# Optimization experiments

Hardware: AMD Instinct MI355X
Metric: run time of the kernel (lower is better)

## Reference

```python
import jax, jax.numpy as jnp
import numpy as np

DIM = 512
HEADS = 8
HEAD_DIM = DIM // HEADS
SCALE = HEAD_DIM ** -0.5
CPB_HIDDEN = 512
N_CLASSES = 2
LN_EPS = 1e-5


def _layernorm(x, g, b):
    m = jnp.mean(x, axis=-1, keepdims=True)
    v = jnp.var(x, axis=-1, keepdims=True)
    return (x - m) / jnp.sqrt(v + LN_EPS) * g + b


def _coord_attention(x, coords, cpb_w1, cpb_b1, cpb_w2, cpb_b2, qkv_w, qkv_b, proj_w, proj_b):
    B, N, C = x.shape
    qkv = (x @ qkv_w + qkv_b).reshape(B, N, 3, HEADS, HEAD_DIM)
    q, k, v = jnp.moveaxis(qkv, 2, 0)  # each (B, N, H, hd)
    attn = jnp.einsum('bnhd,bmhd->bhnm', q * SCALE, k)  # (B, H, N, N)
    rel = coords[:, :, None, :] - coords[:, None, :, :]  # (B, N, N, 2)
    rel = rel / (jnp.linalg.norm(rel, axis=-1, keepdims=True) + 1e-6)
    bias = jax.nn.relu(rel @ cpb_w1 + cpb_b1) @ cpb_w2 + cpb_b2  # (B, N, N, H)
    attn = jax.nn.softmax(attn + jnp.transpose(bias, (0, 3, 1, 2)), axis=-1)
    out = jnp.einsum('bhnm,bmhd->bnhd', attn, v).reshape(B, N, C)
    return out @ proj_w + proj_b


def setup_inputs() -> dict:
    key = jax.random.key(0)
    ks = iter(jax.random.split(key, 32))
    d = {}
    d['h'] = jax.random.normal(next(ks), (1, 400, 1024), dtype=jnp.float32)
    d['coords'] = jax.random.uniform(next(ks), (1, 400, 2), dtype=jnp.float32) * 1000.0
    def lin(kw, kb, fan_in, fan_out):
        w = jax.random.normal(kw, (fan_in, fan_out), dtype=jnp.float32) / np.sqrt(fan_in)
        b = jax.random.normal(kb, (fan_out,), dtype=jnp.float32) * 0.01
        return w, b
    d['fc1_w'], d['fc1_b'] = lin(next(ks), next(ks), 1024, DIM)
    d['cls_token'] = jax.random.normal(next(ks), (1, 1, DIM), dtype=jnp.float32)
    for p in ('l1', 'l2'):
        d[p + '_norm_g'] = jnp.ones((DIM,), jnp.float32)
        d[p + '_norm_b'] = jnp.zeros((DIM,), jnp.float32)
        d[p + '_cpb_w1'], d[p + '_cpb_b1'] = lin(next(ks), next(ks), 2, CPB_HIDDEN)
        d[p + '_cpb_w2'], d[p + '_cpb_b2'] = lin(next(ks), next(ks), CPB_HIDDEN, HEADS)
        d[p + '_qkv_w'], d[p + '_qkv_b'] = lin(next(ks), next(ks), DIM, 3 * DIM)
        d[p + '_proj_w'], d[p + '_proj_b'] = lin(next(ks), next(ks), DIM, DIM)
    d['norm_g'] = jnp.ones((DIM,), jnp.float32)
    d['norm_b'] = jnp.zeros((DIM,), jnp.float32)
    d['fc2_w'], d['fc2_b'] = lin(next(ks), next(ks), DIM, N_CLASSES)
    return d


def reference(h, coords, fc1_w, fc1_b, cls_token,
              l1_norm_g, l1_norm_b, l1_cpb_w1, l1_cpb_b1, l1_cpb_w2, l1_cpb_b2,
              l1_qkv_w, l1_qkv_b, l1_proj_w, l1_proj_b,
              l2_norm_g, l2_norm_b, l2_cpb_w1, l2_cpb_b1, l2_cpb_w2, l2_cpb_b2,
              l2_qkv_w, l2_qkv_b, l2_proj_w, l2_proj_b,
              norm_g, norm_b, fc2_w, fc2_b):
    B, Np, _ = h.shape
    h = jax.nn.relu(h @ fc1_w + fc1_b)  # (B, N, 512)
    side = int(np.ceil(np.sqrt(Np)))
    add = side * side - Np  # pad bag to a perfect square (wrap-around copy)
    h = jnp.concatenate([h, h[:, :add, :]], axis=1)
    coords = jnp.concatenate([coords, coords[:, :add, :]], axis=1)
    cls = jnp.broadcast_to(cls_token, (B, 1, DIM))
    h = jnp.concatenate([cls, h], axis=1)
    coords = jnp.concatenate([jnp.zeros((B, 1, 2), h.dtype), coords], axis=1)
    h = h + _coord_attention(_layernorm(h, l1_norm_g, l1_norm_b), coords,
                             l1_cpb_w1, l1_cpb_b1, l1_cpb_w2, l1_cpb_b2,
                             l1_qkv_w, l1_qkv_b, l1_proj_w, l1_proj_b)
    h = h + _coord_attention(_layernorm(h, l2_norm_g, l2_norm_b), coords,
                             l2_cpb_w1, l2_cpb_b1, l2_cpb_w2, l2_cpb_b2,
                             l2_qkv_w, l2_qkv_b, l2_proj_w, l2_proj_b)
    h = _layernorm(h, norm_g, norm_b)[:, 0]  # CLS token
    return h @ fc2_w + fc2_b  # (B, n_classes)
```

## Files before the change

kernel.cpp:

```cpp
#include <hip/hip_runtime.h>
#include <math.h>

#define NP 401
#define DIM 512
#define LN_EPS 1e-5f
#define ATT_SCALE 0.125f
#define SP 448
#define PLANE (NP * SP)
#define CPB_M 16384
#define TSTRIDE (CPB_M + 64)
#define PQS (401L * 1536)
#define PVS (401L * 512)

template<bool TB, typename LA, typename LB>
__device__ __forceinline__ void gemm64(
    int kBeg, int kEnd, int tid,
    float (*as)[68], float (*bs)[68], float (&acc)[4][4],
    LA&& loadA, LB&& loadB)
{
    float aR[4], bR[4];
    loadA(kBeg, aR);
    loadB(kBeg, bR);
    for (int k0 = kBeg; k0 < kEnd; k0 += 16) {
        const int arow = tid >> 2, aq = tid & 3;
        as[aq * 4 + 0][arow] = aR[0];
        as[aq * 4 + 1][arow] = aR[1];
        as[aq * 4 + 2][arow] = aR[2];
        as[aq * 4 + 3][arow] = aR[3];
        if (!TB) {
            *(float4*)&bs[tid >> 4][(tid & 15) * 4] =
                make_float4(bR[0], bR[1], bR[2], bR[3]);
        } else {
            bs[aq * 4 + 0][arow] = bR[0];
            bs[aq * 4 + 1][arow] = bR[1];
            bs[aq * 4 + 2][arow] = bR[2];
            bs[aq * 4 + 3][arow] = bR[3];
        }
        __syncthreads();
        float nA[4] = {0.f,0.f,0.f,0.f}, nB[4] = {0.f,0.f,0.f,0.f};
        if (k0 + 16 < kEnd) { loadA(k0 + 16, nA); loadB(k0 + 16, nB); }
        const int tx = tid & 15, ty = tid >> 4;
        #pragma unroll
        for (int kk = 0; kk < 16; ++kk) {
            float4 a4 = *(const float4*)&as[kk][ty * 4];
            float4 b4 = *(const float4*)&bs[kk][tx * 4];
            float av[4] = {a4.x, a4.y, a4.z, a4.w};
            float bv[4] = {b4.x, b4.y, b4.z, b4.w};
            #pragma unroll
            for (int r = 0; r < 4; ++r)
                #pragma unroll
                for (int c = 0; c < 4; ++c)
                    acc[r][c] = fmaf(av[r], bv[c], acc[r][c]);
        }
        __syncthreads();
        #pragma unroll
        for (int j = 0; j < 4; ++j) { aR[j] = nA[j]; bR[j] = nB[j]; }
    }
}

__global__ __launch_bounds__(256) void gemm_split_kernel(
    const float* __restrict__ A, int lda,
    const float* __restrict__ B, int ldb,
    float* __restrict__ P, int ldc, long slice,
    int M, int N, int K, int skN)
{
    __shared__ float as[16][68], bs[16][68];
    const int tid = threadIdx.x;
    const int m0 = blockIdx.x * 64, n0 = blockIdx.y * 64;
    const int sk = blockIdx.z;
    const int KS = ((K + skN * 16 - 1) / (skN * 16)) * 16;
    const int kBeg = sk * KS;
    const int kEnd = (kBeg + KS < K) ? kBeg + KS : K;
    float acc[4][4] = {};

    auto loadA = [&](int k0, float r[4]) {
        r[0] = r[1] = r[2] = r[3] = 0.f;
        int gm = m0 + (tid >> 2);
        if (gm >= M) return;
        int gk = k0 + (tid & 3) * 4;
        const float* p = A + (long)gm * lda + gk;
        if (gk + 3 < kEnd) {
            float4 v = *(const float4*)p;
            r[0] = v.x; r[1] = v.y; r[2] = v.z; r[3] = v.w;
        } else {
            #pragma unroll
            for (int j = 0; j < 4; ++j) if (gk + j < kEnd) r[j] = p[j];
        }
    };
    auto loadB = [&](int k0, float r[4]) {
        r[0] = r[1] = r[2] = r[3] = 0.f;
        int gk = k0 + (tid >> 4);
        if (gk >= kEnd) return;
        int gn = n0 + (tid & 15) * 4;
        const float* p = B + (long)gk * ldb + gn;
        float4 v = *(const float4*)p;
        r[0] = v.x; r[1] = v.y; r[2] = v.z; r[3] = v.w;
    };
    if (kBeg < kEnd)
        gemm64<false>(kBeg, kEnd, tid, as, bs, acc, loadA, loadB);

    float* C = P + (long)sk * slice;
    const int tx = tid & 15, ty = tid >> 4;
    #pragma unroll
    for (int r = 0; r < 4; ++r) {
        int m = m0 + ty * 4 + r;
        if (m >= M) continue;
        *(float4*)&C[(long)m * ldc + n0 + tx * 4] =
            make_float4(acc[r][0], acc[r][1], acc[r][2], acc[r][3]);
    }
}

__global__ __launch_bounds__(256) void reduce_kernel(
    const float* __restrict__ P, long slice, int skN,
    const float* __restrict__ bias, float* __restrict__ out,
    int total, int N)
{
    int idx = (blockIdx.x * 256 + threadIdx.x) * 4;
    if (idx >= total) return;
    float4 s = *(const float4*)(P + idx);
    for (int k = 1; k < skN; ++k) {
        float4 p = *(const float4*)(P + (long)k * slice + idx);
        s.x += p.x; s.y += p.y; s.z += p.z; s.w += p.w;
    }
    if (bias) {
        const float4 b = *(const float4*)(bias + (idx % N));
        s.x += b.x; s.y += b.y; s.z += b.z; s.w += b.w;
    }
    *(float4*)(out + idx) = s;
}

__global__ __launch_bounds__(256) void qk_kernel(
    const float* __restrict__ qkv,
    const int* __restrict__ pm, const float* __restrict__ pf,
    const float* __restrict__ T, float* __restrict__ S)
{
    __shared__ float as[16][68], bs[16][68];
    const int tid = threadIdx.x;
    const int m0 = blockIdx.x * 64, n0 = blockIdx.y * 64, h = blockIdx.z;
    float acc[4][4] = {};

    auto loadQ = [&](int k0, float r[4]) {
        int gm = m0 + (tid >> 2);
        if (gm > 400) { r[0]=r[1]=r[2]=r[3]=0.f; return; }
        int gk = k0 + (tid & 3) * 4;
        float4 v = *(const float4*)(qkv + (long)gm * 1536 + h * 64 + gk);
        r[0]=v.x; r[1]=v.y; r[2]=v.z; r[3]=v.w;
    };
    auto loadK = [&](int k0, float r[4]) {
        int gn = n0 + (tid >> 2);
        if (gn > 400) { r[0]=r[1]=r[2]=r[3]=0.f; return; }
        int gk = k0 + (tid & 3) * 4;
        float4 v = *(const float4*)(qkv + (long)gn * 1536 + 512 + h * 64 + gk);
        r[0]=v.x; r[1]=v.y; r[2]=v.z; r[3]=v.w;
    };
    gemm64<true>(0, 64, tid, as, bs, acc, loadQ, loadK);

    const int tx = tid & 15, ty = tid >> 4;
    const float* Tt = T + (long)h * TSTRIDE;
    float* Sp = S + (long)h * PLANE;
    #pragma unroll
    for (int r = 0; r < 4; ++r) {
        int i = m0 + ty * 4 + r;
        if (i > 400) continue;
        #pragma unroll
        for (int c = 0; c < 4; ++c) {
            int j = n0 + tx * 4 + c;
            if (j > 400) continue;
            int id = i * 416 + j;
            int mm = pm[id];
            float fr = pf[id];
            float t0 = Tt[mm], t1 = Tt[mm + 1];
            Sp[(long)i * SP + j] =
                fmaf(acc[r][c], ATT_SCALE, fmaf(fr, t1 - t0, t0));
        }
    }
}

__global__ __launch_bounds__(256) void softmax_kernel(float* __restrict__ S)
{
    int r = blockIdx.x * 4 + (threadIdx.x >> 6);
    if (r >= 3208) return;
    int hh = r / 401, i = r - hh * 401;
    float* row = S + (long)hh * PLANE + (long)i * SP;
    int lane = threadIdx.x & 63;
    float v[7], mx = -INFINITY;
    #pragma unroll
    for (int j = 0; j < 7; ++j) {
        int c = lane + j * 64;
        v[j] = (c < NP) ? row[c] : -INFINITY;
        mx = fmaxf(mx, v[j]);
    }
    #pragma unroll
    for (int off = 32; off > 0; off >>= 1)
        mx = fmaxf(mx, __shfl_xor(mx, off));
    float s = 0.f;
    #pragma unroll
    for (int j = 0; j < 7; ++j) {
        v[j] = (lane + j * 64 < NP) ? __expf(v[j] - mx) : 0.f;
        s += v[j];
    }
    #pragma unroll
    for (int off = 32; off > 0; off >>= 1)
        s += __shfl_xor(s, off);
    float inv = 1.f / s;
    #pragma unroll
    for (int j = 0; j < 7; ++j) {
        int c = lane + j * 64;
        if (c < NP) row[c] = v[j] * inv;
    }
}

__global__ __launch_bounds__(256) void pv_kernel(
    const float* __restrict__ S, const float* __restrict__ qkv,
    float* __restrict__ Pv)
{
    __shared__ float as[16][68], bs[16][68];
    const int tid = threadIdx.x;
    const int m0 = blockIdx.x * 64;
    const int h = blockIdx.z >> 2, sk = blockIdx.z & 3;
    const int kBeg = sk * 112;
    const int kEnd = (kBeg + 112 < NP) ? kBeg + 112 : NP;
    float acc[4][4] = {};

    auto loadA = [&](int k0, float r[4]) {
        r[0] = r[1] = r[2] = r[3] = 0.f;
        int gm = m0 + (tid >> 2);
        if (gm > 400) return;
        int gk = k0 + (tid & 3) * 4;
        const float* p = S + (long)h * PLANE + (long)gm * SP + gk;
        if (gk + 3 < kEnd) {
            float4 v = *(const float4*)p;
            r[0]=v.x; r[1]=v.y; r[2]=v.z; r[3]=v.w;
        } else {
            #pragma unroll
            for (int j = 0; j < 4; ++j) if (gk + j < kEnd) r[j] = p[j];
        }
    };
    auto loadB = [&](int k0, float r[4]) {
        r[0] = r[1] = r[2] = r[3] = 0.f;
        int key = k0 + (tid >> 4);
        if (key >= kEnd) return;
        int d = (tid & 15) * 4;
        float4 v = *(const float4*)(qkv + (long)key * 1536 + 1024 + h * 64 + d);
        r[0]=v.x; r[1]=v.y; r[2]=v.z; r[3]=v.w;
    };
    gemm64<false>(kBeg, kEnd, tid, as, bs, acc, loadA, loadB);

    float* C = Pv + (long)sk * PVS;
    const int tx = tid & 15, ty = tid >> 4;
    #pragma unroll
    for (int r = 0; r < 4; ++r) {
        int m = m0 + ty * 4 + r;
        if (m > 400) continue;
        *(float4*)&C[(long)m * 512 + h * 64 + tx * 4] =
            make_float4(acc[r][0], acc[r][1], acc[r][2], acc[r][3]);
    }
}

__global__ __launch_bounds__(256) void proj_kernel(
    const float* __restrict__ att, const float* __restrict__ projw,
    float* __restrict__ Pp)
{
    __shared__ float as[16][68], bs[16][68];
    const int tid = threadIdx.x;
    const int m0 = blockIdx.x * 64, n0 = blockIdx.y * 64, sk = blockIdx.z;
    const int kBeg = sk * 64, kEnd = kBeg + 64;
    float acc[4][4] = {};

    auto loadA = [&](int k0, float r[4]) {
        r[0] = r[1] = r[2] = r[3] = 0.f;
        int gm = m0 + (tid >> 2);
        if (gm > 400) return;
        int gk = k0 + (tid & 3) * 4;
        float4 v = *(const float4*)(att + (long)gm * 512 + gk);
        r[0]=v.x; r[1]=v.y; r[2]=v.z; r[3]=v.w;
    };
    auto loadB = [&](int k0, float r[4]) {
        int gk = k0 + (tid >> 4);
        int gn = n0 + (tid & 15) * 4;
        float4 v = *(const float4*)(projw + (long)gk * 512 + gn);
        r[0]=v.x; r[1]=v.y; r[2]=v.z; r[3]=v.w;
    };
    gemm64<false>(kBeg, kEnd, tid, as, bs, acc, loadA, loadB);

    float* C = Pp + (long)sk * PVS;
    const int tx = tid & 15, ty = tid >> 4;
    #pragma unroll
    for (int r = 0; r < 4; ++r) {
        int m = m0 + ty * 4 + r;
        if (m > 400) continue;
        *(float4*)&C[(long)m * 512 + n0 + tx * 4] =
            make_float4(acc[r][0], acc[r][1], acc[r][2], acc[r][3]);
    }
}

__global__ __launch_bounds__(256) void rowfuse_kernel(
    const float* __restrict__ P, long slice, int skN, int rowOff,
    const float* __restrict__ bias, int doRelu,
    const float* __restrict__ resid, const float* __restrict__ cls,
    float* __restrict__ h0,
    const float* __restrict__ g, const float* __restrict__ b,
    float* __restrict__ xln)
{
    const int r = blockIdx.x, t = threadIdx.x;
    float v0, v1;
    if (cls && r == 0) {
        v0 = cls[t]; v1 = cls[t + 256];
    } else {
        const float* p = P + (long)(r - rowOff) * DIM;
        v0 = bias[t]; v1 = bias[t + 256];
        for (int k = 0; k < skN; ++k) {
            v0 += p[(long)k * slice + t];
            v1 += p[(long)k * slice + t + 256];
        }
        if (resid) {
            v0 += resid[(long)r * DIM + t];
            v1 += resid[(long)r * DIM + t + 256];
        }
        if (doRelu) { v0 = fmaxf(v0, 0.f); v1 = fmaxf(v1, 0.f); }
    }
    h0[(long)r * DIM + t] = v0;
    h0[(long)r * DIM + t + 256] = v1;

    float s = v0 + v1, sq = v0 * v0 + v1 * v1;
    #pragma unroll
    for (int off = 32; off > 0; off >>= 1) {
        s += __shfl_down(s, off);
        sq += __shfl_down(sq, off);
    }
    __shared__ float ps[4], pq[4];
    int w = t >> 6, lane = t & 63;
    if (lane == 0) { ps[w] = s; pq[w] = sq; }
    __syncthreads();
    float Sm = ps[0] + ps[1] + ps[2] + ps[3];
    float Q = pq[0] + pq[1] + pq[2] + pq[3];
    float mean = Sm * (1.f / DIM);
    float var = Q * (1.f / DIM) - mean * mean;
    float inv = rsqrtf(var + LN_EPS);
    xln[(long)r * DIM + t]       = (v0 - mean) * inv * g[t] + b[t];
    xln[(long)r * DIM + t + 256] = (v1 - mean) * inv * g[t + 256] + b[t + 256];
}

__global__ __launch_bounds__(256) void cls_decode_kernel(
    const float* __restrict__ qkv,
    const int* __restrict__ pm, const float* __restrict__ pf,
    const float* __restrict__ T,
    float* __restrict__ cms, float* __restrict__ cpv)
{
    const int h = blockIdx.x, c = blockIdx.y, tid = threadIdx.x;
    const int kBeg = c * 64;
    __shared__ float q0[64], scraw[64], p[64], red[4][64], rr[2];

    if (tid < 64) q0[tid] = qkv[h * 64 + tid];
    __syncthreads();

    {
        int k = tid >> 2, q = tid & 3;
        int j = kBeg + k;
        float dot = 0.f;
        if (j < NP) {
            const float* kp = qkv + (long)j * 1536 + 512 + h * 64 + q * 16;
            const float* qp = q0 + q * 16;
            #pragma unroll
            for (int d = 0; d < 16; d += 4) {
                float4 kv = *(const float4*)(kp + d);
                float4 qq = *(const float4*)(qp + d);
                dot = fmaf(qq.x, kv.x, dot);
                dot = fmaf(qq.y, kv.y, dot);
                dot = fmaf(qq.z, kv.z, dot);
                dot = fmaf(qq.w, kv.w, dot);
            }
        }
        dot += __shfl_down(dot, 2);
        dot += __shfl_down(dot, 1);
        if (q == 0) scraw[k] = dot;
    }
    __syncthreads();

    if (tid < 64) {
        int j = kBeg + tid;
        float s;
        if (j < NP) {
            int mm = pm[j];
            float fr = pf[j];
            const float* Tt = T + (long)h * TSTRIDE;
            float t0 = Tt[mm], t1 = Tt[mm + 1];
            s = fmaf(scraw[tid], ATT_SCALE, fmaf(fr, t1 - t0, t0));
        } else {
            s = -INFINITY;
        }
        float m = s;
        #pragma unroll
        for (int off = 32; off > 0; off >>= 1)
            m = fmaxf(m, __shfl_xor(m, off));
        float e = (j < NP) ? __expf(s - m) : 0.f;
        float sum = e;
        #pragma unroll
        for (int off = 32; off > 0; off >>= 1)
            sum += __shfl_xor(sum, off);
        p[tid] = e;
        if (tid == 0) { rr[0] = m; rr[1] = sum; }
    }
    __syncthreads();

    {
        int w = tid >> 6, d = tid & 63;
        float acc = 0.f;
        for (int k = w; k < 64; k += 4) {
            int j = kBeg + k;
            if (j >= NP) break;
            acc = fmaf(p[k], qkv[(long)j * 1536 + 1024 + h * 64 + d], acc);
        }
        red[w][d] = acc;
    }
    __syncthreads();
    if (tid < 64) {
        cpv[((long)h * 7 + c) * 64 + tid] =
            red[0][tid] + red[1][tid] + red[2][tid] + red[3][tid];
        if (tid == 0) {
            cms[(h * 7 + c) * 2 + 0] = rr[0];
            cms[(h * 7 + c) * 2 + 1] = rr[1];
        }
    }
}

__global__ __launch_bounds__(256) void cls_proj_kernel(
    const float* __restrict__ cms, const float* __restrict__ cpv,
    const float* __restrict__ projw, const float* __restrict__ projb,
    float* __restrict__ proj0)
{
    __shared__ float av[512], red[4][64];
    const int b = blockIdx.x, tid = threadIdx.x;
    for (int d = tid; d < 512; d += 256) {
        int h = d >> 6, dd = d & 63;
        float M = -INFINITY;
        #pragma unroll
        for (int c = 0; c < 7; ++c)
            M = fmaxf(M, cms[(h * 7 + c) * 2]);
        float S = 0.f, acc = 0.f;
        #pragma unroll
        for (int c = 0; c < 7; ++c) {
            float e = __expf(cms[(h * 7 + c) * 2] - M);
            S += cms[(h * 7 + c) * 2 + 1] * e;
            acc += cpv[((long)h * 7 + c) * 64 + dd] * e;
        }
        av[d] = acc / S;
    }
    __syncthreads();
    int g = tid >> 6, n = b * 64 + (tid & 63);
    float acc = 0.f;
    for (int k = g * 128; k < g * 128 + 128; ++k)
        acc = fmaf(av[k], projw[(long)k * 512 + n], acc);
    red[g][tid & 63] = acc;
    __syncthreads();
    if (tid < 64)
        proj0[b * 64 + tid] = red[0][tid] + red[1][tid] + red[2][tid]
                              + red[3][tid] + projb[b * 64 + tid];
}

__global__ __launch_bounds__(256) void cls_out_kernel(
    const float* __restrict__ h0, const float* __restrict__ proj0,
    const float* __restrict__ g, const float* __restrict__ b,
    const float* __restrict__ fc2w, const float* __restrict__ fc2b,
    float* __restrict__ out)
{
    const int t = threadIdx.x;
    float v0 = h0[t] + proj0[t];
    float v1 = h0[t + 256] + proj0[t + 256];
    float s = v0 + v1, sq = v0 * v0 + v1 * v1;
    #pragma unroll
    for (int off = 32; off > 0; off >>= 1) {
        s += __shfl_down(s, off);
        sq += __shfl_down(sq, off);
    }
    __shared__ float ps[4], pq[4], pc0[4], pc1[4];
    int w = t >> 6, lane = t & 63;
    if (lane == 0) { ps[w] = s; pq[w] = sq; }
    __syncthreads();
    float Sm = ps[0] + ps[1] + ps[2] + ps[3];
    float Q = pq[0] + pq[1] + pq[2] + pq[3];
    float mean = Sm * (1.f / DIM);
    float var = Q * (1.f / DIM) - mean * mean;
    float inv = rsqrtf(var + LN_EPS);
    float n0 = (v0 - mean) * inv * g[t] + b[t];
    float n1 = (v1 - mean) * inv * g[t + 256] + b[t + 256];
    float c0 = n0 * fc2w[t * 2]     + n1 * fc2w[(t + 256) * 2];
    float c1 = n0 * fc2w[t * 2 + 1] + n1 * fc2w[(t + 256) * 2 + 1];
    #pragma unroll
    for (int off = 32; off > 0; off >>= 1) {
        c0 += __shfl_down(c0, off);
        c1 += __shfl_down(c1, off);
    }
    if (lane == 0) { pc0[w] = c0; pc1[w] = c1; }
    __syncthreads();
    if (t == 0) {
        out[0] = pc0[0] + pc0[1] + pc0[2] + pc0[3] + fc2b[0];
        out[1] = pc1[0] + pc1[1] + pc1[2] + pc1[3] + fc2b[1];
    }
}

__global__ __launch_bounds__(256) void mega_kernel(
    const float* __restrict__ hin, const float* __restrict__ fc1_w,
    const float* __restrict__ w1_0, const float* __restrict__ b1_0,
    const float* __restrict__ w2_0, const float* __restrict__ b2_0,
    const float* __restrict__ w1_1, const float* __restrict__ b1_1,
    const float* __restrict__ w2_1, const float* __restrict__ b2_1,
    const float* __restrict__ coords,
    float* __restrict__ Pp, float* __restrict__ T,
    int* __restrict__ pm, float* __restrict__ pf)
{
    __shared__ float smem[2176];
    float (*as)[68] = (float(*)[68])smem;
    float (*bs)[68] = (float(*)[68])(smem + 1088);
    float (*red)[64][8] = (float(*)[64][8])smem;
    const int bid = blockIdx.x, tid = threadIdx.x;

    if (bid < 896) {
        int sk = bid / 56, rem = bid % 56;
        int m0 = (rem % 7) * 64, n0 = (rem / 7) * 64;
        int kBeg = sk * 64, kEnd = kBeg + 64;
        float acc[4][4] = {};
        auto loadA = [&](int k0, float r[4]) {
            r[0]=r[1]=r[2]=r[3]=0.f;
            int gm = m0 + (tid >> 2);
            if (gm >= 400) return;
            int gk = k0 + (tid & 3) * 4;
            float4 v = *(const float4*)(hin + (long)gm * 1024 + gk);
            r[0]=v.x; r[1]=v.y; r[2]=v.z; r[3]=v.w;
        };
        auto loadB = [&](int k0, float r[4]) {
            int gk = k0 + (tid >> 4);
            int gn = n0 + (tid & 15) * 4;
            float4 v = *(const float4*)(fc1_w + (long)gk * 512 + gn);
            r[0]=v.x; r[1]=v.y; r[2]=v.z; r[3]=v.w;
        };
        gemm64<false>(kBeg, kEnd, tid, as, bs, acc, loadA, loadB);
        float* C = Pp + (long)sk * PVS;
        const int tx = tid & 15, ty = tid >> 4;
        #pragma unroll
        for (int r = 0; r < 4; ++r) {
            int m = m0 + ty * 4 + r;
            if (m >= 400) continue;
            *(float4*)&C[(long)m * 512 + n0 + tx * 4] =
                make_float4(acc[r][0], acc[r][1], acc[r][2], acc[r][3]);
        }
    } else if (bid < 1410) {
        int tb = bid - 896;
        int z = tb / 257, ab = tb % 257;
        const float* w1 = z ? w1_1 : w1_0;
        const float* b1 = z ? b1_1 : b1_0;
        const float* w2 = z ? w2_1 : w2_0;
        const float* b2 = z ? b2_1 : b2_0;
        const int lane = tid & 63, wv = tid >> 6;
        float ca = 0.f, sa = 0.f;
        if (ab != 256) {
            float th = fmaf((float)(ab * 64 + lane),
                            (float)(2.0 * M_PI / CPB_M), -(float)M_PI);
            sincosf(th, &sa, &ca);
        } else if (lane == 0) {
            sincosf((float)M_PI, &sa, &ca);
        }
        float a8[8] = {};
        const int kbeg = wv * 128;
        #pragma unroll 4
        for (int k = kbeg; k < kbeg + 128; ++k) {
            float hk = fmaxf(fmaf(ca, w1[k],
                                  fmaf(sa, w1[512 + k], b1[k])), 0.f);
            #pragma unroll
            for (int h2 = 0; h2 < 8; ++h2)
                a8[h2] = fmaf(hk, w2[k * 8 + h2], a8[h2]);
        }
        #pragma unroll
        for (int h2 = 0; h2 < 8; ++h2) red[wv][lane][h2] = a8[h2];
        __syncthreads();
        if (tid < 64) {
            int aidx = ab * 64 + tid;
            #pragma unroll
            for (int h2 = 0; h2 < 8; ++h2)
                T[(long)(z * 8 + h2) * TSTRIDE + aidx] =
                    red[0][tid][h2] + red[1][tid][h2] +
                    red[2][tid][h2] + red[3][tid][h2] + b2[h2];
        }
    } else {
        int p = (bid - 1410) * 256 + tid;
        if (p < NP * NP) {
            int i = p / NP, j = p - i * NP;
            float xi = (i == 0) ? 0.f : coords[(i - 1) * 2];
            float yi = (i == 0) ? 0.f : coords[(i - 1) * 2 + 1];
            float xj = (j == 0) ? 0.f : coords[(j - 1) * 2];
            float yj = (j == 0) ? 0.f : coords[(j - 1) * 2 + 1];
            float rx = xi - xj, ry = yi - yj;
            int mm; float fr;
            if (rx == 0.f && ry == 0.f) {
                mm = CPB_M + 1; fr = 0.f;
            } else {
                float x = (atan2f(ry, rx) + 3.14159265358979f)
                          * (float)(CPB_M / (2.0 * M_PI));
                int mi = (int)x;
                fr = x - (float)mi;
                mm = (mi >= CPB_M) ? mi - CPB_M : mi;
            }
            pm[i * 416 + j] = mm;
            pf[i * 416 + j] = fr;
        }
    }
}

extern "C" void kernel_launch(void* const* d_in, const int* in_sizes, int n_in,
                              void* d_out, int out_size, void* d_ws, size_t ws_size,
                              hipStream_t stream)
{
    const float* coords = (const float*)d_in[1];
    float* ws = (float*)d_ws;
    float* h0   = ws;                    ws += 401L * 512;
    float* xln  = ws;                    ws += 401L * 512;
    float* S    = ws;                    ws += 8L * PLANE;
    float* T    = ws;                    ws += 16L * TSTRIDE;
    int*   pm   = (int*)ws;              ws += 401L * 416;
    float* pf   = ws;                    ws += 401L * 416;
    float* Pq   = ws;                    ws += 4L * PQS;
    float* qkv  = ws;                    ws += 401L * 1536;
    float* Pv   = ws;                    ws += 4L * PVS;
    float* att  = ws;                    ws += 401L * 512;
    float* Pp   = ws;                    ws += 16L * PVS;
    float* proj0 = ws;                   ws += 512;
    float* cms  = ws;                    ws += 8L * 7 * 2;
    float* cpv  = ws;                    ws += 8L * 7 * 64;

    mega_kernel<<<2039, 256, 0, stream>>>(
        (const float*)d_in[0], (const float*)d_in[2],
        (const float*)d_in[7],  (const float*)d_in[8],
        (const float*)d_in[9],  (const float*)d_in[10],
        (const float*)d_in[17], (const float*)d_in[18],
        (const float*)d_in[19], (const float*)d_in[20],
        coords, Pp, T, pm, pf);

    rowfuse_kernel<<<401, 256, 0, stream>>>(
        Pp, PVS, 16, 1, (const float*)d_in[3], 1, nullptr,
        (const float*)d_in[4], h0,
        (const float*)d_in[5], (const float*)d_in[6], xln);

    gemm_split_kernel<<<dim3(7, 24, 4), 256, 0, stream>>>(
        xln, 512, (const float*)d_in[11], 1536, Pq, 1536, PQS,
        401, 1536, 512, 4);
    reduce_kernel<<<602, 256, 0, stream>>>(
        Pq, PQS, 4, (const float*)d_in[12], qkv, 401 * 1536, 1536);
    qk_kernel<<<dim3(7, 7, 8), 256, 0, stream>>>(qkv, pm, pf, T, S);
    softmax_kernel<<<802, 256, 0, stream>>>(S);
    pv_kernel<<<dim3(7, 1, 32), 256, 0, stream>>>(S, qkv, Pv);
    reduce_kernel<<<201, 256, 0, stream>>>(
        Pv, PVS, 4, nullptr, att, 401 * 512, 512);
    proj_kernel<<<dim3(7, 8, 8), 256, 0, stream>>>(
        att, (const float*)d_in[13], Pp);
    rowfuse_kernel<<<401, 256, 0, stream>>>(
        Pp, PVS, 8, 0, (const float*)d_in[14], 0, h0, nullptr, h0,
        (const float*)d_in[15], (const float*)d_in[16], xln);

    gemm_split_kernel<<<dim3(7, 24, 4), 256, 0, stream>>>(
        xln, 512, (const float*)d_in[21], 1536, Pq, 1536, PQS,
        401, 1536, 512, 4);
    reduce_kernel<<<602, 256, 0, stream>>>(
        Pq, PQS, 4, (const float*)d_in[22], qkv, 401 * 1536, 1536);
    cls_decode_kernel<<<dim3(8, 7), 256, 0, stream>>>(
        qkv, pm, pf, T + 8L * TSTRIDE, cms, cpv);
    cls_proj_kernel<<<8, 256, 0, stream>>>(
        cms, cpv, (const float*)d_in[23], (const float*)d_in[24], proj0);
    cls_out_kernel<<<1, 256, 0, stream>>>(
        h0, proj0, (const float*)d_in[25], (const float*)d_in[26],
        (const float*)d_in[27], (const float*)d_in[28], (float*)d_out);
}
```

Baseline: 250.4 us.

## Fuse layer-1 attention into flash-style kernel and merge CLS tail kernels

Replaces the separate QK, softmax, split-K PV and reduce kernels of the first attention layer with one online-softmax flash kernel. Each block handles 32 queries for one head, streams K/V tiles through shared memory and writes normalized output directly, so the score matrix and the PV partials never go to global memory. The three CLS-only kernels for the second layer are merged into one single-block kernel that loops over heads and then does projection, layernorm and classifier. This cuts launches and memory traffic, but the flash grid has only 104 blocks and the tail runs serially on one block, so parallelism drops.

```diff
diff --git a/kernel.cpp b/kernel.cpp
--- a/kernel.cpp
+++ b/kernel.cpp
@@ -5,8 +5,6 @@
 #define DIM 512
 #define LN_EPS 1e-5f
 #define ATT_SCALE 0.125f
-#define SP 448
-#define PLANE (NP * SP)
 #define CPB_M 16384
 #define TSTRIDE (CPB_M + 64)
 #define PQS (401L * 1536)
@@ -129,131 +127,162 @@
     *(float4*)(out + idx) = s;
 }
 
-__global__ __launch_bounds__(256) void qk_kernel(
+__global__ __launch_bounds__(256) void flash_kernel(
     const float* __restrict__ qkv,
     const int* __restrict__ pm, const float* __restrict__ pf,
-    const float* __restrict__ T, float* __restrict__ S)
-{
-    __shared__ float as[16][68], bs[16][68];
+    const float* __restrict__ T, float* __restrict__ att)
+{
+    __shared__ float qsT[64 * 32];
+    __shared__ float kT[64 * 68];
+    __shared__ float vs[64 * 68];
+    __shared__ float psT[64 * 34];
     const int tid = threadIdx.x;
-    const int m0 = blockIdx.x * 64, n0 = blockIdx.y * 64, h = blockIdx.z;
-    float acc[4][4] = {};
-
-    auto loadQ = [&](int k0, float r[4]) {
-        int gm = m0 + (tid >> 2);
-        if (gm > 400) { r[0]=r[1]=r[2]=r[3]=0.f; return; }
-        int gk = k0 + (tid & 3) * 4;
-        float4 v = *(const float4*)(qkv + (long)gm * 1536 + h * 64 + gk);
-        r[0]=v.x; r[1]=v.y; r[2]=v.z; r[3]=v.w;
-    };
-    auto loadK = [&](int k0, float r[4]) {
-        int gn = n0 + (tid >> 2);
-        if (gn > 400) { r[0]=r[1]=r[2]=r[3]=0.f; return; }
-        int gk = k0 + (tid & 3) * 4;
-        float4 v = *(const float4*)(qkv + (long)gn * 1536 + 512 + h * 64 + gk);
-        r[0]=v.x; r[1]=v.y; r[2]=v.z; r[3]=v.w;
-    };
-    gemm64<true>(0, 64, tid, as, bs, acc, loadQ, loadK);
-
+    const int m0 = blockIdx.x * 32, h = blockIdx.y;
     const int tx = tid & 15, ty = tid >> 4;
+    const int i0 = ty * 2;
+
+    {
+        int i = tid >> 3, dq = (tid & 7) * 8;
+        int gm = m0 + i;
+        float4 a = make_float4(0, 0, 0, 0), b = make_float4(0, 0, 0, 0);
+        if (gm <= 400) {
+            const float* p = qkv + (long)gm * 1536 + h * 64 + dq;
+            a = *(const float4*)p;
+            b = *(const float4*)(p + 4);
+        }
+        qsT[(dq + 0) * 32 + i] = a.x;
+        qsT[(dq + 1) * 32 + i] = a.y;
+        qsT[(dq + 2) * 32 + i] = a.z;
+        qsT[(dq + 3) * 32 + i] = a.w;
+        qsT[(dq + 4) * 32 + i] = b.x;
+        qsT[(dq + 5) * 32 + i] = b.y;
+        qsT[(dq + 6) * 32 + i] = b.z;
+        qsT[(dq + 7) * 32 + i] = b.w;
+    }
+
+    float O[2][4] = {{0.f,0.f,0.f,0.f},{0.f,0.f,0.f,0.f}};
+    float mr[2] = {-INFINITY, -INFINITY};
+    float lr[2] = {0.f, 0.f};
     const float* Tt = T + (long)h * TSTRIDE;
-    float* Sp = S + (long)h * PLANE;
+    const int ig0 = (m0 + i0     <= 400) ? m0 + i0     : 400;
+    const int ig1 = (m0 + i0 + 1 <= 400) ? m0 + i0 + 1 : 400;
+
+    for (int c = 0; c < 7; ++c) {
+        const int kBeg = c * 64;
+        __syncthreads();
+        {
+            int j = tid >> 2, dq = (tid & 3) * 16;
+            int gj = kBeg + j;
+            float4 k4[4], v4[4];
+            #pragma unroll
+            for (int q = 0; q < 4; ++q) {
+                k4[q] = make_float4(0, 0, 0, 0);
+                v4[q] = make_float4(0, 0, 0, 0);
+            }
+            if (gj <= 400) {
+                const float* kp = qkv + (long)gj * 1536 + 512 + h * 64 + dq;
+                const float* vp = kp + 512;
+                #pragma unroll
+                for (int q = 0; q < 4; ++q) {
+                    k4[q] = *(const float4*)(kp + q * 4);
+                    v4[q] = *(const float4*)(vp + q * 4);
+                }
+            }
+            #pragma unroll
+            for (int q = 0; q < 4; ++q) {
+                kT[(dq + q * 4 + 0) * 68 + j] = k4[q].x;
+                kT[(dq + q * 4 + 1) * 68 + j] = k4[q].y;
+                kT[(dq + q * 4 + 2) * 68 + j] = k4[q].z;
+                kT[(dq + q * 4 + 3) * 68 + j] = k4[q].w;
+                *(float4*)&vs[j * 68 + dq + q * 4] = v4[q];
+            }
+        }
+        __syncthreads();
+
+        float s0[4] = {0.f,0.f,0.f,0.f}, s1[4] = {0.f,0.f,0.f,0.f};
+        #pragma unroll
+        for (int d = 0; d < 64; ++d) {
+            float2 q2 = *(const float2*)&qsT[d * 32 + i0];
+            float4 k4 = *(const float4*)&kT[d * 68 + tx * 4];
+            s0[0] = fmaf(q2.x, k4.x, s0[0]);
+            s0[1] = fmaf(q2.x, k4.y, s0[1]);
+            s0[2] = fmaf(q2.x, k4.z, s0[2]);
+            s0[3] = fmaf(q2.x, k4.w, s0[3]);
+            s1[0] = fmaf(q2.y, k4.x, s1[0]);
+            s1[1] = fmaf(q2.y, k4.y, s1[1]);
+            s1[2] = fmaf(q2.y, k4.z, s1[2]);
+            s1[3] = fmaf(q2.y, k4.w, s1[3]);
+        }
+        #pragma unroll
+        for (int cc = 0; cc < 4; ++cc) {
+            int jg = kBeg + tx * 4 + cc;
+            if (jg <= 400) {
+                int id0 = ig0 * 416 + jg, id1 = ig1 * 416 + jg;
+                int ma = pm[id0], mb = pm[id1];
+                float fa = pf[id0], fb = pf[id1];
+                float a0 = Tt[ma], a1 = Tt[ma + 1];
+                float b0 = Tt[mb], b1 = Tt[mb + 1];
+                s0[cc] = fmaf(s0[cc], ATT_SCALE, fmaf(fa, a1 - a0, a0));
+                s1[cc] = fmaf(s1[cc], ATT_SCALE, fmaf(fb, b1 - b0, b0));
+            } else {
+                s0[cc] = -INFINITY;
+                s1[cc] = -INFINITY;
+            }
+        }
+        #pragma unroll
+        for (int r = 0; r < 2; ++r) {
+            float* s = r ? s1 : s0;
+            float cmax = fmaxf(fmaxf(s[0], s[1]), fmaxf(s[2], s[3]));
+            cmax = fmaxf(cmax, __shfl_xor(cmax, 1));
+            cmax = fmaxf(cmax, __shfl_xor(cmax, 2));
+            cmax = fmaxf(cmax, __shfl_xor(cmax, 4));
+            cmax = fmaxf(cmax, __shfl_xor(cmax, 8));
+            float mn = fmaxf(mr[r], cmax);
+            float al = __expf(mr[r] - mn);
+            float rs = 0.f;
+            #pragma unroll
+            for (int cc = 0; cc < 4; ++cc) {
+                float e = __expf(s[cc] - mn);
+                s[cc] = e;
+                rs += e;
+            }
+            rs += __shfl_xor(rs, 1);
+            rs += __shfl_xor(rs, 2);
+            rs += __shfl_xor(rs, 4);
+            rs += __shfl_xor(rs, 8);
+            lr[r] = lr[r] * al + rs;
+            mr[r] = mn;
+            #pragma unroll
+            for (int cc = 0; cc < 4; ++cc) {
+                O[r][cc] *= al;
+                psT[(tx * 4 + cc) * 34 + i0 + r] = s[cc];
+            }
+        }
+        __syncthreads();
+
+        #pragma unroll 4
+        for (int j = 0; j < 64; ++j) {
+            float2 p2 = *(const float2*)&psT[j * 34 + i0];
+            float4 v4 = *(const float4*)&vs[j * 68 + tx * 4];
+            O[0][0] = fmaf(p2.x, v4.x, O[0][0]);
+            O[0][1] = fmaf(p2.x, v4.y, O[0][1]);
+            O[0][2] = fmaf(p2.x, v4.z, O[0][2]);
+            O[0][3] = fmaf(p2.x, v4.w, O[0][3]);
+            O[1][0] = fmaf(p2.y, v4.x, O[1][0]);
+            O[1][1] = fmaf(p2.y, v4.y, O[1][1]);
+            O[1][2] = fmaf(p2.y, v4.z, O[1][2]);
+            O[1][3] = fmaf(p2.y, v4.w, O[1][3]);
+        }
+    }
+
     #pragma unroll
-    for (int r = 0; r < 4; ++r) {
-        int i = m0 + ty * 4 + r;
-        if (i > 400) continue;
-        #pragma unroll
-        for (int c = 0; c < 4; ++c) {
-            int j = n0 + tx * 4 + c;
-            if (j > 400) continue;
-            int id = i * 416 + j;
-            int mm = pm[id];
-            float fr = pf[id];
-            float t0 = Tt[mm], t1 = Tt[mm + 1];
-            Sp[(long)i * SP + j] =
-                fmaf(acc[r][c], ATT_SCALE, fmaf(fr, t1 - t0, t0));
-        }
-    }
-}
-
-__global__ __launch_bounds__(256) void softmax_kernel(float* __restrict__ S)
-{
-    int r = blockIdx.x * 4 + (threadIdx.x >> 6);
-    if (r >= 3208) return;
-    int hh = r / 401, i = r - hh * 401;
-    float* row = S + (long)hh * PLANE + (long)i * SP;
-    int lane = threadIdx.x & 63;
-    float v[7], mx = -INFINITY;
-    #pragma unroll
-    for (int j = 0; j < 7; ++j) {
-        int c = lane + j * 64;
-        v[j] = (c < NP) ? row[c] : -INFINITY;
-        mx = fmaxf(mx, v[j]);
-    }
-    #pragma unroll
-    for (int off = 32; off > 0; off >>= 1)
-        mx = fmaxf(mx, __shfl_xor(mx, off));
-    float s = 0.f;
-    #pragma unroll
-    for (int j = 0; j < 7; ++j) {
-        v[j] = (lane + j * 64 < NP) ? __expf(v[j] - mx) : 0.f;
-        s += v[j];
-    }
-    #pragma unroll
-    for (int off = 32; off > 0; off >>= 1)
-        s += __shfl_xor(s, off);
-    float inv = 1.f / s;
-    #pragma unroll
-    for (int j = 0; j < 7; ++j) {
-        int c = lane + j * 64;
-        if (c < NP) row[c] = v[j] * inv;
-    }
-}
-
-__global__ __launch_bounds__(256) void pv_kernel(
-    const float* __restrict__ S, const float* __restrict__ qkv,
-    float* __restrict__ Pv)
-{
-    __shared__ float as[16][68], bs[16][68];
-    const int tid = threadIdx.x;
-    const int m0 = blockIdx.x * 64;
-    const int h = blockIdx.z >> 2, sk = blockIdx.z & 3;
-    const int kBeg = sk * 112;
-    const int kEnd = (kBeg + 112 < NP) ? kBeg + 112 : NP;
-    float acc[4][4] = {};
-
-    auto loadA = [&](int k0, float r[4]) {
-        r[0] = r[1] = r[2] = r[3] = 0.f;
-        int gm = m0 + (tid >> 2);
-        if (gm > 400) return;
-        int gk = k0 + (tid & 3) * 4;
-        const float* p = S + (long)h * PLANE + (long)gm * SP + gk;
-        if (gk + 3 < kEnd) {
-            float4 v = *(const float4*)p;
-            r[0]=v.x; r[1]=v.y; r[2]=v.z; r[3]=v.w;
-        } else {
-            #pragma unroll
-            for (int j = 0; j < 4; ++j) if (gk + j < kEnd) r[j] = p[j];
-        }
-    };
-    auto loadB = [&](int k0, float r[4]) {
-        r[0] = r[1] = r[2] = r[3] = 0.f;
-        int key = k0 + (tid >> 4);
-        if (key >= kEnd) return;
-        int d = (tid & 15) * 4;
-        float4 v = *(const float4*)(qkv + (long)key * 1536 + 1024 + h * 64 + d);
-        r[0]=v.x; r[1]=v.y; r[2]=v.z; r[3]=v.w;
-    };
-    gemm64<false>(kBeg, kEnd, tid, as, bs, acc, loadA, loadB);
-
-    float* C = Pv + (long)sk * PVS;
-    const int tx = tid & 15, ty = tid >> 4;
-    #pragma unroll
-    for (int r = 0; r < 4; ++r) {
-        int m = m0 + ty * 4 + r;
-        if (m > 400) continue;
-        *(float4*)&C[(long)m * 512 + h * 64 + tx * 4] =
-            make_float4(acc[r][0], acc[r][1], acc[r][2], acc[r][3]);
+    for (int r = 0; r < 2; ++r) {
+        int ig = m0 + i0 + r;
+        if (ig > 400) continue;
+        float inv = 1.f / lr[r];
+        *(float4*)&att[(long)ig * 512 + h * 64 + tx * 4] =
+            make_float4(O[r][0] * inv, O[r][1] * inv,
+                        O[r][2] * inv, O[r][3] * inv);
     }
 }
 
@@ -341,132 +370,86 @@
     xln[(long)r * DIM + t + 256] = (v1 - mean) * inv * g[t + 256] + b[t + 256];
 }
 
-__global__ __launch_bounds__(256) void cls_decode_kernel(
+__global__ __launch_bounds__(256) void cls_tail_kernel(
     const float* __restrict__ qkv,
     const int* __restrict__ pm, const float* __restrict__ pf,
     const float* __restrict__ T,
-    float* __restrict__ cms, float* __restrict__ cpv)
-{
-    const int h = blockIdx.x, c = blockIdx.y, tid = threadIdx.x;
-    const int kBeg = c * 64;
-    __shared__ float q0[64], scraw[64], p[64], red[4][64], rr[2];
-
-    if (tid < 64) q0[tid] = qkv[h * 64 + tid];
-    __syncthreads();
-
-    {
-        int k = tid >> 2, q = tid & 3;
-        int j = kBeg + k;
-        float dot = 0.f;
-        if (j < NP) {
-            const float* kp = qkv + (long)j * 1536 + 512 + h * 64 + q * 16;
-            const float* qp = q0 + q * 16;
-            #pragma unroll
-            for (int d = 0; d < 16; d += 4) {
-                float4 kv = *(const float4*)(kp + d);
-                float4 qq = *(const float4*)(qp + d);
-                dot = fmaf(qq.x, kv.x, dot);
-                dot = fmaf(qq.y, kv.y, dot);
-                dot = fmaf(qq.z, kv.z, dot);
-                dot = fmaf(qq.w, kv.w, dot);
-            }
-        }
-        dot += __shfl_down(dot, 2);
-        dot += __shfl_down(dot, 1);
-        if (q == 0) scraw[k] = dot;
-    }
-    __syncthreads();
-
-    if (tid < 64) {
-        int j = kBeg + tid;
-        float s;
-        if (j < NP) {
-            int mm = pm[j];
-            float fr = pf[j];
-            const float* Tt = T + (long)h * TSTRIDE;
-            float t0 = Tt[mm], t1 = Tt[mm + 1];
-            s = fmaf(scraw[tid], ATT_SCALE, fmaf(fr, t1 - t0, t0));
-        } else {
-            s = -INFINITY;
-        }
-        float m = s;
-        #pragma unroll
-        for (int off = 32; off > 0; off >>= 1)
-            m = fmaxf(m, __shfl_xor(m, off));
-        float e = (j < NP) ? __expf(s - m) : 0.f;
-        float sum = e;
-        #pragma unroll
-        for (int off = 32; off > 0; off >>= 1)
-            sum += __shfl_xor(sum, off);
-        p[tid] = e;
-        if (tid == 0) { rr[0] = m; rr[1] = sum; }
-    }
-    __syncthreads();
-
-    {
-        int w = tid >> 6, d = tid & 63;
-        float acc = 0.f;
-        for (int k = w; k < 64; k += 4) {
-            int j = kBeg + k;
-            if (j >= NP) break;
-            acc = fmaf(p[k], qkv[(long)j * 1536 + 1024 + h * 64 + d], acc);
-        }
-        red[w][d] = acc;
-    }
-    __syncthreads();
-    if (tid < 64) {
-        cpv[((long)h * 7 + c) * 64 + tid] =
-            red[0][tid] + red[1][tid] + red[2][tid] + red[3][tid];
-        if (tid == 0) {
-            cms[(h * 7 + c) * 2 + 0] = rr[0];
-            cms[(h * 7 + c) * 2 + 1] = rr[1];
-        }
-    }
-}
-
-__global__ __launch_bounds__(256) void cls_proj_kernel(
-    const float* __restrict__ cms, const float* __restrict__ cpv,
     const float* __restrict__ projw, const float* __restrict__ projb,
-    float* __restrict__ proj0)
-{
-    __shared__ float av[512], red[4][64];
-    const int b = blockIdx.x, tid = threadIdx.x;
-    for (int d = tid; d < 512; d += 256) {
-        int h = d >> 6, dd = d & 63;
-        float M = -INFINITY;
-        #pragma unroll
-        for (int c = 0; c < 7; ++c)
-            M = fmaxf(M, cms[(h * 7 + c) * 2]);
-        float S = 0.f, acc = 0.f;
-        #pragma unroll
-        for (int c = 0; c < 7; ++c) {
-            float e = __expf(cms[(h * 7 + c) * 2] - M);
-            S += cms[(h * 7 + c) * 2 + 1] * e;
-            acc += cpv[((long)h * 7 + c) * 64 + dd] * e;
-        }
-        av[d] = acc / S;
-    }
-    __syncthreads();
-    int g = tid >> 6, n = b * 64 + (tid & 63);
-    float acc = 0.f;
-    for (int k = g * 128; k < g * 128 + 128; ++k)
-        acc = fmaf(av[k], projw[(long)k * 512 + n], acc);
-    red[g][tid & 63] = acc;
-    __syncthreads();
-    if (tid < 64)
-        proj0[b * 64 + tid] = red[0][tid] + red[1][tid] + red[2][tid]
-                              + red[3][tid] + projb[b * 64 + tid];
-}
-
-__global__ __launch_bounds__(256) void cls_out_kernel(
-    const float* __restrict__ h0, const float* __restrict__ proj0,
+    const float* __restrict__ h0,
     const float* __restrict__ g, const float* __restrict__ b,
     const float* __restrict__ fc2w, const float* __restrict__ fc2b,
     float* __restrict__ out)
 {
-    const int t = threadIdx.x;
-    float v0 = h0[t] + proj0[t];
-    float v1 = h0[t + 256] + proj0[t + 256];
+    const int tid = threadIdx.x;
+    const int w = tid >> 6, lane = tid & 63;
+    __shared__ float q0[64], sc[512], av[512], red[4][64], rr[8];
+
+    for (int h = 0; h < 8; ++h) {
+        if (tid < 64) q0[tid] = qkv[h * 64 + tid];
+        __syncthreads();
+        const float* Tt = T + (long)h * TSTRIDE;
+        #pragma unroll
+        for (int jj = 0; jj < 2; ++jj) {
+            int j = tid + jj * 256;
+            if (j < NP) {
+                const float* kp = qkv + (long)j * 1536 + 512 + h * 64;
+                float dot = 0.f;
+                #pragma unroll
+                for (int d = 0; d < 64; d += 4) {
+                    float4 kv = *(const float4*)(kp + d);
+                    float4 qq = *(const float4*)(q0 + d);
+                    dot = fmaf(qq.x, kv.x, dot);
+                    dot = fmaf(qq.y, kv.y, dot);
+                    dot = fmaf(qq.z, kv.z, dot);
+                    dot = fmaf(qq.w, kv.w, dot);
+                }
+                int mm = pm[j];
+                float fr = pf[j];
+                float t0 = Tt[mm], t1 = Tt[mm + 1];
+                sc[j] = fmaf(dot, ATT_SCALE, fmaf(fr, t1 - t0, t0));
+            } else if (j < 512) {
+                sc[j] = -INFINITY;
+            }
+        }
+        __syncthreads();
+        float mx = fmaxf(sc[tid], sc[tid + 256]);
+        #pragma unroll
+        for (int off = 32; off > 0; off >>= 1)
+            mx = fmaxf(mx, __shfl_xor(mx, off));
+        if (lane == 0) rr[w] = mx;
+        __syncthreads();
+        float M = fmaxf(fmaxf(rr[0], rr[1]), fmaxf(rr[2], rr[3]));
+        float e0 = (tid < NP) ? __expf(sc[tid] - M) : 0.f;
+        float e1 = (tid + 256 < NP) ? __expf(sc[tid + 256] - M) : 0.f;
+        float s = e0 + e1;
+        #pragma unroll
+        for (int off = 32; off > 0; off >>= 1)
+            s += __shfl_xor(s, off);
+        if (lane == 0) rr[4 + w] = s;
+        __syncthreads();
+        float inv = 1.f / (rr[4] + rr[5] + rr[6] + rr[7]);
+        sc[tid] = e0 * inv;
+        sc[tid + 256] = e1 * inv;
+        __syncthreads();
+        float acc = 0.f;
+        for (int j = w; j < NP; j += 4)
+            acc = fmaf(sc[j], qkv[(long)j * 1536 + 1024 + h * 64 + lane], acc);
+        red[w][lane] = acc;
+        __syncthreads();
+        if (tid < 64)
+            av[h * 64 + tid] =
+                red[0][tid] + red[1][tid] + red[2][tid] + red[3][tid];
+        __syncthreads();
+    }
+
+    float a0 = projb[tid], a1 = projb[tid + 256];
+    #pragma unroll 8
+    for (int k = 0; k < 512; ++k) {
+        float avk = av[k];
+        a0 = fmaf(avk, projw[(long)k * 512 + tid], a0);
+        a1 = fmaf(avk, projw[(long)k * 512 + tid + 256], a1);
+    }
+    float v0 = h0[tid] + a0, v1 = h0[tid + 256] + a1;
     float s = v0 + v1, sq = v0 * v0 + v1 * v1;
     #pragma unroll
     for (int off = 32; off > 0; off >>= 1) {
@@ -474,7 +457,6 @@
         sq += __shfl_down(sq, off);
     }
     __shared__ float ps[4], pq[4], pc0[4], pc1[4];
-    int w = t >> 6, lane = t & 63;
     if (lane == 0) { ps[w] = s; pq[w] = sq; }
     __syncthreads();
     float Sm = ps[0] + ps[1] + ps[2] + ps[3];
@@ -482,10 +464,10 @@
     float mean = Sm * (1.f / DIM);
     float var = Q * (1.f / DIM) - mean * mean;
     float inv = rsqrtf(var + LN_EPS);
-    float n0 = (v0 - mean) * inv * g[t] + b[t];
-    float n1 = (v1 - mean) * inv * g[t + 256] + b[t + 256];
-    float c0 = n0 * fc2w[t * 2]     + n1 * fc2w[(t + 256) * 2];
-    float c1 = n0 * fc2w[t * 2 + 1] + n1 * fc2w[(t + 256) * 2 + 1];
+    float n0 = (v0 - mean) * inv * g[tid] + b[tid];
+    float n1 = (v1 - mean) * inv * g[tid + 256] + b[tid + 256];
+    float c0 = n0 * fc2w[tid * 2]     + n1 * fc2w[(tid + 256) * 2];
+    float c1 = n0 * fc2w[tid * 2 + 1] + n1 * fc2w[(tid + 256) * 2 + 1];
     #pragma unroll
     for (int off = 32; off > 0; off >>= 1) {
         c0 += __shfl_down(c0, off);
@@ -493,7 +475,7 @@
     }
     if (lane == 0) { pc0[w] = c0; pc1[w] = c1; }
     __syncthreads();
-    if (t == 0) {
+    if (tid == 0) {
         out[0] = pc0[0] + pc0[1] + pc0[2] + pc0[3] + fc2b[0];
         out[1] = pc1[0] + pc1[1] + pc1[2] + pc1[3] + fc2b[1];
     }
@@ -614,18 +596,13 @@
     float* ws = (float*)d_ws;
     float* h0   = ws;                    ws += 401L * 512;
     float* xln  = ws;                    ws += 401L * 512;
-    float* S    = ws;                    ws += 8L * PLANE;
     float* T    = ws;                    ws += 16L * TSTRIDE;
     int*   pm   = (int*)ws;              ws += 401L * 416;
     float* pf   = ws;                    ws += 401L * 416;
     float* Pq   = ws;                    ws += 4L * PQS;
     float* qkv  = ws;                    ws += 401L * 1536;
-    float* Pv   = ws;                    ws += 4L * PVS;
     float* att  = ws;                    ws += 401L * 512;
     float* Pp   = ws;                    ws += 16L * PVS;
-    float* proj0 = ws;                   ws += 512;
-    float* cms  = ws;                    ws += 8L * 7 * 2;
-    float* cpv  = ws;                    ws += 8L * 7 * 64;
 
     mega_kernel<<<2039, 256, 0, stream>>>(
         (const float*)d_in[0], (const float*)d_in[2],
@@ -645,11 +622,7 @@
         401, 1536, 512, 4);
     reduce_kernel<<<602, 256, 0, stream>>>(
         Pq, PQS, 4, (const float*)d_in[12], qkv, 401 * 1536, 1536);
-    qk_kernel<<<dim3(7, 7, 8), 256, 0, stream>>>(qkv, pm, pf, T, S);
-    softmax_kernel<<<802, 256, 0, stream>>>(S);
-    pv_kernel<<<dim3(7, 1, 32), 256, 0, stream>>>(S, qkv, Pv);
-    reduce_kernel<<<201, 256, 0, stream>>>(
-        Pv, PVS, 4, nullptr, att, 401 * 512, 512);
+    flash_kernel<<<dim3(13, 8), 256, 0, stream>>>(qkv, pm, pf, T, att);
     proj_kernel<<<dim3(7, 8, 8), 256, 0, stream>>>(
         att, (const float*)d_in[13], Pp);
     rowfuse_kernel<<<401, 256, 0, stream>>>(
@@ -661,11 +634,9 @@
         401, 1536, 512, 4);
     reduce_kernel<<<602, 256, 0, stream>>>(
         Pq, PQS, 4, (const float*)d_in[22], qkv, 401 * 1536, 1536);
-    cls_decode_kernel<<<dim3(8, 7), 256, 0, stream>>>(
-        qkv, pm, pf, T + 8L * TSTRIDE, cms, cpv);
-    cls_proj_kernel<<<8, 256, 0, stream>>>(
-        cms, cpv, (const float*)d_in[23], (const float*)d_in[24], proj0);
-    cls_out_kernel<<<1, 256, 0, stream>>>(
-        h0, proj0, (const float*)d_in[25], (const float*)d_in[26],
+    cls_tail_kernel<<<1, 256, 0, stream>>>(
+        qkv, pm, pf, T + 8L * TSTRIDE,
+        (const float*)d_in[23], (const float*)d_in[24], h0,
+        (const float*)d_in[25], (const float*)d_in[26],
         (const float*)d_in[27], (const float*)d_in[28], (float*)d_out);
 }
```

Result: slower. 514.1 us (+105.3%).
